# Optimization experiments

Measured on AMD Instinct MI355X. Metric: run time of the kernel, lower is better.

## Reference

```python
import jax, jax.numpy as jnp
import numpy as np

V, BLK, H, D, L = 32000, 1024, 16, 1024, 3
HD = D // H  # 64
B, T = 4, 1024


def _layernorm(x, g, b, eps=1e-5):
    mu = jnp.mean(x, axis=-1, keepdims=True)
    var = jnp.mean(jnp.square(x - mu), axis=-1, keepdims=True)
    return (x - mu) * jax.lax.rsqrt(var + eps) * g + b


def setup_inputs() -> dict:
    key = jax.random.key(0)
    ks = jax.random.split(key, 32)
    s = 0.02
    inp = {}
    inp["idx"] = jax.random.randint(ks[0], (B, T), 0, V)
    inp["target"] = jax.random.randint(ks[1], (B, T), 0, V)
    inp["tok_emb"] = jax.random.normal(ks[2], (V, D), jnp.float32) * s
    inp["pos_emb"] = jax.random.normal(ks[3], (BLK, D), jnp.float32) * s
    inp["wq"] = jax.random.normal(ks[4], (L, H, D, HD), jnp.float32) * s
    inp["wk"] = jax.random.normal(ks[5], (L, H, D, HD), jnp.float32) * s
    inp["wv"] = jax.random.normal(ks[6], (L, H, D, HD), jnp.float32) * s
    inp["wproj"] = jax.random.normal(ks[7], (L, D, D), jnp.float32) * s
    inp["bproj"] = jnp.zeros((L, D), jnp.float32)
    inp["ln1_g"] = jnp.ones((L, D), jnp.float32)
    inp["ln1_b"] = jnp.zeros((L, D), jnp.float32)
    inp["ln2_g"] = jnp.ones((L, D), jnp.float32)
    inp["ln2_b"] = jnp.zeros((L, D), jnp.float32)
    inp["w1"] = jax.random.normal(ks[8], (L, D, 4 * D), jnp.float32) * s
    inp["b1"] = jnp.zeros((L, 4 * D), jnp.float32)
    inp["w2"] = jax.random.normal(ks[9], (L, 4 * D, D), jnp.float32) * s
    inp["b2"] = jnp.zeros((L, D), jnp.float32)
    inp["lnf_g"] = jnp.ones((D,), jnp.float32)
    inp["lnf_b"] = jnp.zeros((D,), jnp.float32)
    inp["wlm"] = jax.random.normal(ks[10], (D, V), jnp.float32) * s
    inp["blm"] = jnp.zeros((V,), jnp.float32)
    return inp


def reference(idx, target, tok_emb, pos_emb, wq, wk, wv, wproj, bproj,
              ln1_g, ln1_b, ln2_g, ln2_b, w1, b1, w2, b2,
              lnf_g, lnf_b, wlm, blm):
    Bb, Tt = idx.shape
    x = tok_emb[idx] + pos_emb[:Tt]  # [B,T,D]
    mask = jnp.tril(jnp.ones((Tt, Tt), dtype=bool))  # causal
    scale = D ** -0.5  # NOTE: source scales by n_embd**-0.5, not head_size**-0.5
    for l in range(L):
        xn = _layernorm(x, ln1_g[l], ln1_b[l])
        q = jnp.einsum('btd,hde->bhte', xn, wq[l])
        k = jnp.einsum('btd,hde->bhte', xn, wk[l])
        v = jnp.einsum('btd,hde->bhte', xn, wv[l])
        scores = jnp.einsum('bhte,bhse->bhts', q, k) * scale
        scores = jnp.where(mask, scores, -jnp.inf)
        attn = jax.nn.softmax(scores, axis=-1)
        o = jnp.einsum('bhts,bhse->bhte', attn, v)
        o = o.transpose(0, 2, 1, 3).reshape(Bb, Tt, D)  # concat heads
        x = x + o @ wproj[l] + bproj[l]
        xn2 = _layernorm(x, ln2_g[l], ln2_b[l])
        h = jax.nn.relu(xn2 @ w1[l] + b1[l])
        x = x + h @ w2[l] + b2[l]
    x = _layernorm(x, lnf_g, lnf_b)
    logits = x @ wlm + blm  # [B,T,V]
    logp = jax.nn.log_softmax(logits, axis=-1)
    nll = -jnp.take_along_axis(logp, target[..., None], axis=-1)[..., 0]
    loss = jnp.mean(nll)
    return logits, loss
```

## Files before the change

kernel.cpp:

```cpp
#include <hip/hip_runtime.h>
#include <math.h>

#define Dn   1024
#define Hn   16
#define HDn  64
#define Tn   1024
#define Bn   4
#define Vn   32000
#define Ln   3
#define NT   (Bn*Tn)

typedef __attribute__((ext_vector_type(8))) short bf16x8;
typedef __attribute__((ext_vector_type(4))) float f32x4;

__device__ __forceinline__ float b2f(unsigned short u) {
  union { float f; unsigned int i; } c; c.i = ((unsigned int)u) << 16; return c.f;
}
__device__ __forceinline__ unsigned short f2b(float f) {
  union { float f; unsigned int i; } c; c.f = f;
  unsigned int r = (c.i + 0x7FFFu + ((c.i >> 16) & 1u)) >> 16;
  return (unsigned short)r;
}

#define GLOAD_LDS16(g, l) __builtin_amdgcn_global_load_lds( \
    (const __attribute__((address_space(1))) void*)(g),     \
    (__attribute__((address_space(3))) void*)(l), 16, 0, 0)

#define SBAR()  __builtin_amdgcn_s_barrier()
#define SCHED() __builtin_amdgcn_sched_barrier(0)

__global__ __launch_bounds__(256) void embed_kernel(
    const int* __restrict__ idx, const float* __restrict__ tok,
    const float* __restrict__ pos, float* __restrict__ x) {
  int row = blockIdx.x;
  int t = row & (Tn - 1);
  int token = idx[row];
  const float4* tp = (const float4*)(tok + (size_t)token * Dn);
  const float4* pp = (const float4*)(pos + (size_t)t * Dn);
  float4* xp = (float4*)(x + (size_t)row * Dn);
  int i = threadIdx.x;
  float4 a = tp[i], b = pp[i];
  xp[i] = make_float4(a.x + b.x, a.y + b.y, a.z + b.z, a.w + b.w);
}

__global__ __launch_bounds__(256) void ln_kernel(
    const float* __restrict__ x, const float* __restrict__ g,
    const float* __restrict__ b, unsigned short* __restrict__ y) {
  int row = blockIdx.x;
  const float4* xr = (const float4*)(x + (size_t)row * Dn);
  __shared__ float red[4];
  int lane = threadIdx.x & 63, w = threadIdx.x >> 6;

  float4 v = xr[threadIdx.x];
  float s = v.x + v.y + v.z + v.w;
  #pragma unroll
  for (int o = 32; o > 0; o >>= 1) s += __shfl_down(s, o, 64);
  if (lane == 0) red[w] = s;
  __syncthreads();
  float mu = (red[0] + red[1] + red[2] + red[3]) * (1.0f / Dn);
  __syncthreads();

  float dx = v.x - mu, dy = v.y - mu, dz = v.z - mu, dw = v.w - mu;
  float ss = dx*dx + dy*dy + dz*dz + dw*dw;
  #pragma unroll
  for (int o = 32; o > 0; o >>= 1) ss += __shfl_down(ss, o, 64);
  if (lane == 0) red[w] = ss;
  __syncthreads();
  float var = (red[0] + red[1] + red[2] + red[3]) * (1.0f / Dn);
  float inv = rsqrtf(var + 1e-5f);

  float4 gv = ((const float4*)g)[threadIdx.x];
  float4 bv = ((const float4*)b)[threadIdx.x];
  ushort4 o4;
  o4.x = f2b(dx*inv*gv.x + bv.x);
  o4.y = f2b(dy*inv*gv.y + bv.y);
  o4.z = f2b(dz*inv*gv.z + bv.z);
  o4.w = f2b(dw*inv*gv.w + bv.w);
  ((ushort4*)(y + (size_t)row * Dn))[threadIdx.x] = o4;
}

__global__ __launch_bounds__(256) void wcast_kernel(
    const float* __restrict__ src, unsigned short* __restrict__ dst,
    int K, int M, long long bsk, long long bsh) {
  __shared__ float t[32][33];
  int m0 = blockIdx.x << 5, k0 = blockIdx.y << 5;
  int tid = threadIdx.x;
  int ml = tid & 31, kl = tid >> 5;
  #pragma unroll
  for (int p = 0; p < 4; ++p) {
    int k = k0 + kl + p * 8;
    int m = m0 + ml;
    t[ml][kl + p * 8] = src[(size_t)k * bsk + (size_t)(m >> 6) * bsh + (m & 63)];
  }
  __syncthreads();
  int kl2 = tid & 31, ml2 = tid >> 5;
  #pragma unroll
  for (int p = 0; p < 4; ++p) {
    int m = m0 + ml2 + p * 8;
    int k = k0 + kl2;
    dst[(size_t)m * K + k] = f2b(t[ml2 + p * 8][kl2]);
  }
}

__global__ __launch_bounds__(256) void mm_bf16(
    const unsigned short* __restrict__ A, const unsigned short* __restrict__ BT,
    const float* __restrict__ bias, const float* __restrict__ res,
    float* __restrict__ Cf, unsigned short* __restrict__ Ch,
    int N, int K, int M, int relu) {
  __shared__ __align__(16) unsigned short As[2][128 * 32];
  __shared__ __align__(16) unsigned short Bs[2][128 * 32];
  const int tid = threadIdx.x;
  const int lane = tid & 63, w = tid >> 6, g = lane >> 4;
  const int wr = w >> 1, wc = w & 1;
  const int n0 = blockIdx.x << 7, m0 = blockIdx.y << 7;

  f32x4 acc[4][4];
  #pragma unroll
  for (int i = 0; i < 4; ++i)
    #pragma unroll
    for (int j = 0; j < 4; ++j)
      acc[i][j] = (f32x4){0.f, 0.f, 0.f, 0.f};

  const int beta0 = w * 2048 + lane * 16;
  const int beta1 = beta0 + 1024;
  const int r0 = beta0 >> 6, u0 = (beta0 >> 4) & 3;
  const int r1 = beta1 >> 6, u1 = (beta1 >> 4) & 3;
  const int ks0 = u0 ^ ((r0 >> 1) & 3);
  const int ks1 = u1 ^ ((r1 >> 1) & 3);
  const unsigned short* a_g0 = A + (size_t)(n0 + r0) * K + ks0 * 8;
  const unsigned short* a_g1 = A + (size_t)(n0 + r1) * K + ks1 * 8;
  const unsigned short* b_g0 = BT + (size_t)(m0 + r0) * K + ks0 * 8;
  const unsigned short* b_g1 = BT + (size_t)(m0 + r1) * K + ks1 * 8;

  int a_off[4], b_off[4];
  #pragma unroll
  for (int f = 0; f < 4; ++f) {
    int row = wr * 64 + f * 16 + (lane & 15);
    a_off[f] = row * 64 + ((g ^ ((row >> 1) & 3)) << 4);
    int col = wc * 64 + f * 16 + (lane & 15);
    b_off[f] = col * 64 + ((g ^ ((col >> 1) & 3)) << 4);
  }

#define MM_STAGE(buf, kk) do {                                   \
    GLOAD_LDS16(a_g0 + (kk), As[buf] + w * 1024);                \
    GLOAD_LDS16(a_g1 + (kk), As[buf] + w * 1024 + 512);          \
    GLOAD_LDS16(b_g0 + (kk), Bs[buf] + w * 1024);                \
    GLOAD_LDS16(b_g1 + (kk), Bs[buf] + w * 1024 + 512); } while (0)

#define MM_COMPUTE(buf) do {                                     \
    bf16x8 af[4], bfr[4];                                        \
    _Pragma("unroll")                                            \
    for (int f = 0; f < 4; ++f) {                                \
      af[f]  = *(const bf16x8*)((const char*)As[buf] + a_off[f]);\
      bfr[f] = *(const bf16x8*)((const char*)Bs[buf] + b_off[f]);\
    }                                                            \
    _Pragma("unroll")                                            \
    for (int i = 0; i < 4; ++i)                                  \
      _Pragma("unroll")                                          \
      for (int j = 0; j < 4; ++j)                                \
        acc[i][j] = __builtin_amdgcn_mfma_f32_16x16x32_bf16(af[i], bfr[j], acc[i][j], 0, 0, 0); } while (0)

  MM_STAGE(0, 0);
  int cur = 0;
  for (int k0 = 0; k0 < K - 32; k0 += 32) {
    MM_STAGE(cur ^ 1, k0 + 32);
    asm volatile("s_waitcnt vmcnt(4)" ::: "memory");
    SCHED(); SBAR(); SCHED();
    MM_COMPUTE(cur);
    SCHED(); SBAR(); SCHED();
    cur ^= 1;
  }
  asm volatile("s_waitcnt vmcnt(0)" ::: "memory");
  SCHED(); SBAR(); SCHED();
  MM_COMPUTE(cur);

  #pragma unroll
  for (int fc = 0; fc < 4; ++fc) {
    int colg = m0 + wc * 64 + fc * 16 + (lane & 15);
    float bz = bias ? bias[colg] : 0.f;
    #pragma unroll
    for (int fr = 0; fr < 4; ++fr) {
      #pragma unroll
      for (int i = 0; i < 4; ++i) {
        int rowg = n0 + wr * 64 + fr * 16 + (g << 2) + i;
        float v = acc[fr][fc][i] + bz;
        if (res) v += res[(size_t)rowg * M + colg];
        if (relu) v = fmaxf(v, 0.f);
        if (Cf) Cf[(size_t)rowg * M + colg] = v;
        else    Ch[(size_t)rowg * M + colg] = f2b(v);
      }
    }
  }
#undef MM_STAGE
#undef MM_COMPUTE
}

template<int OMODE>
__global__ __launch_bounds__(512) void mm512_bf16(
    const unsigned short* __restrict__ A, const unsigned short* __restrict__ BT,
    const float* __restrict__ bias, const float* __restrict__ res,
    float* __restrict__ Cf, unsigned short* __restrict__ Ch,
    float* __restrict__ rowsum, int N, int K, int M, int relu) {
  __shared__ __align__(16) unsigned short As[2][128 * 32];
  __shared__ __align__(16) unsigned short Bs[2][256 * 32];
  __shared__ float rsum2[OMODE == 4 ? 128 * 4 : 4];
  const int tid = threadIdx.x;
  const int lane = tid & 63, w = tid >> 6, g = lane >> 4;
  const int wr = w >> 2, wc = w & 3;
  const int n0 = blockIdx.x << 7, m0 = blockIdx.y << 8;

  f32x4 acc[4][4];
  #pragma unroll
  for (int i = 0; i < 4; ++i)
    #pragma unroll
    for (int j = 0; j < 4; ++j)
      acc[i][j] = (f32x4){0.f, 0.f, 0.f, 0.f};

  const int arow = tid >> 2, au = tid & 3;
  const int aks = au ^ ((arow >> 1) & 3);
  const unsigned short* a_g = A + (size_t)(n0 + arow) * K + aks * 8;
  const int brow1 = (tid + 512) >> 2;
  const int bks0 = au ^ ((arow >> 1) & 3);
  const int bks1 = au ^ ((brow1 >> 1) & 3);
  const unsigned short* b_g0 = BT + (size_t)(m0 + arow) * K + bks0 * 8;
  const unsigned short* b_g1 = BT + (size_t)(m0 + brow1) * K + bks1 * 8;

  int a_off[4], b_off[4];
  #pragma unroll
  for (int f = 0; f < 4; ++f) {
    int row = wr * 64 + f * 16 + (lane & 15);
    a_off[f] = row * 64 + ((g ^ ((row >> 1) & 3)) << 4);
    int col = wc * 64 + f * 16 + (lane & 15);
    b_off[f] = col * 64 + ((g ^ ((col >> 1) & 3)) << 4);
  }

#define MM5_STAGE(buf, kk) do {                                  \
    GLOAD_LDS16(a_g + (kk), As[buf] + tid * 8);                  \
    GLOAD_LDS16(b_g0 + (kk), Bs[buf] + tid * 8);                 \
    GLOAD_LDS16(b_g1 + (kk), Bs[buf] + (tid + 512) * 8); } while (0)

#define MM5_COMPUTE(buf) do {                                    \
    bf16x8 af[4], bfr[4];                                        \
    _Pragma("unroll")                                            \
    for (int f = 0; f < 4; ++f) {                                \
      af[f]  = *(const bf16x8*)((const char*)As[buf] + a_off[f]);\
      bfr[f] = *(const bf16x8*)((const char*)Bs[buf] + b_off[f]);\
    }                                                            \
    _Pragma("unroll")                                            \
    for (int i = 0; i < 4; ++i)                                  \
      _Pragma("unroll")                                          \
      for (int j = 0; j < 4; ++j)                                \
        acc[i][j] = __builtin_amdgcn_mfma_f32_16x16x32_bf16(af[i], bfr[j], acc[i][j], 0, 0, 0); } while (0)

  MM5_STAGE(0, 0);
  int cur = 0;
  for (int k0 = 0; k0 < K - 32; k0 += 32) {
    MM5_STAGE(cur ^ 1, k0 + 32);
    asm volatile("s_waitcnt vmcnt(3)" ::: "memory");
    SCHED(); SBAR(); SCHED();
    MM5_COMPUTE(cur);
    SCHED(); SBAR(); SCHED();
    cur ^= 1;
  }
  asm volatile("s_waitcnt vmcnt(0)" ::: "memory");
  SCHED(); SBAR(); SCHED();
  MM5_COMPUTE(cur);

  if (OMODE == 0) {
    #pragma unroll
    for (int fc = 0; fc < 4; ++fc) {
      int colg = m0 + wc * 64 + fc * 16 + (lane & 15);
      float bz = bias ? bias[colg] : 0.f;
      #pragma unroll
      for (int fr = 0; fr < 4; ++fr) {
        #pragma unroll
        for (int i = 0; i < 4; ++i) {
          int rowg = n0 + wr * 64 + fr * 16 + (g << 2) + i;
          float v = acc[fr][fc][i] + bz;
          if (res) v += res[(size_t)rowg * M + colg];
          if (relu) v = fmaxf(v, 0.f);
          if (Cf) Cf[(size_t)rowg * M + colg] = v;
          else    Ch[(size_t)rowg * M + colg] = f2b(v);
        }
      }
    }
  } else if (OMODE == 3) {
    unsigned short* kb  = Ch + (size_t)NT * Dn;
    unsigned short* vtb = Ch + 2 * (size_t)NT * Dn;
    #pragma unroll
    for (int fc = 0; fc < 4; ++fc) {
      int colg = m0 + wc * 64 + fc * 16 + (lane & 15);
      int sel = colg >> 10, hh = (colg >> 6) & 15, e = colg & 63;
      #pragma unroll
      for (int fr = 0; fr < 4; ++fr) {
        int rowg0 = n0 + wr * 64 + fr * 16 + (g << 2);
        int b = rowg0 >> 10, t0 = rowg0 & 1023;
        if (sel == 2) {
          ushort4 pk;
          pk.x = f2b(acc[fr][fc][0]); pk.y = f2b(acc[fr][fc][1]);
          pk.z = f2b(acc[fr][fc][2]); pk.w = f2b(acc[fr][fc][3]);
          *(ushort4*)&vtb[(((size_t)(b * 16 + hh) * 64) + e) * 1024 + t0] = pk;
        } else {
          unsigned short* dst = (sel == 0) ? Ch : kb;
          #pragma unroll
          for (int i = 0; i < 4; ++i)
            dst[(((size_t)(b * 16 + hh) * 1024) + t0 + i) * 64 + e] = f2b(acc[fr][fc][i]);
        }
      }
    }
  } else {
    #pragma unroll
    for (int fr = 0; fr < 4; ++fr) {
      #pragma unroll
      for (int i = 0; i < 4; ++i) {
        int rloc = wr * 64 + fr * 16 + (g << 2) + i;
        int rowg = n0 + rloc;
        float es = 0.f;
        #pragma unroll
        for (int fc = 0; fc < 4; ++fc) {
          int colg = m0 + wc * 64 + fc * 16 + (lane & 15);
          float v = acc[fr][fc][i] + bias[colg];
          __builtin_nontemporal_store(v, &Cf[(size_t)rowg * M + colg]);
          es += __expf(v);
        }
        es += __shfl_xor(es, 1); es += __shfl_xor(es, 2);
        es += __shfl_xor(es, 4); es += __shfl_xor(es, 8);
        if ((lane & 15) == 0) rsum2[rloc * 4 + wc] = es;
      }
    }
    __syncthreads();
    if (tid < 128)
      atomicAdd(&rowsum[n0 + tid],
                rsum2[tid * 4 + 0] + rsum2[tid * 4 + 1] +
                rsum2[tid * 4 + 2] + rsum2[tid * 4 + 3]);
  }
#undef MM5_STAGE
#undef MM5_COMPUTE
}

__global__ __launch_bounds__(256) void fattn_kernel(
    const unsigned short* __restrict__ qg, const unsigned short* __restrict__ kg,
    const unsigned short* __restrict__ vtg, unsigned short* __restrict__ ob) {
  const int bid = blockIdx.x;
  const int qt = bid & 15, bh = bid >> 4;
  const int b = bh >> 4, h = bh & 15;
  const int tid = threadIdx.x, lane = tid & 63, w = tid >> 6, g = lane >> 4;

  __shared__ __align__(16) unsigned short Ks[2][64 * 64];
  __shared__ __align__(16) unsigned short Vs[2][64 * 64];
  __shared__ __align__(16) unsigned short Pb[4][16 * 64];

  const unsigned short* kbase = kg + (size_t)bh * Tn * HDn;
  const unsigned short* vbase = vtg + (size_t)bh * HDn * Tn;

  const int qrow = qt * 64 + w * 16 + (lane & 15);
  const unsigned short* qptr = qg + ((size_t)bh * Tn + qrow) * HDn;
  bf16x8 qf0 = *(const bf16x8*)(qptr + g * 8);
  bf16x8 qf1 = *(const bf16x8*)(qptr + 32 + g * 8);

  f32x4 accO[4];
  #pragma unroll
  for (int dt = 0; dt < 4; ++dt) accO[dt] = (f32x4){0.f, 0.f, 0.f, 0.f};
  float mrun[4] = {-1e30f, -1e30f, -1e30f, -1e30f};
  float lrun[4] = {0.f, 0.f, 0.f, 0.f};

  const float scale = 0.03125f;
  const int qout0 = qt * 64 + w * 16 + 4 * g;

  unsigned short* pb = &Pb[w][0];
  const int nsteps = qt + 1;

#define FA_STAGE(buf, s0_) do {                                              \
    _Pragma("unroll")                                                        \
    for (int r = 0; r < 2; ++r) {                                            \
      int c = tid + 256 * r;                                                 \
      int srow = c >> 3, u = c & 7;                                          \
      GLOAD_LDS16(kbase + (size_t)((s0_) + srow) * HDn + ((u ^ (srow & 7)) * 8), Ks[buf] + c * 8); \
    }                                                                        \
    _Pragma("unroll")                                                        \
    for (int r = 0; r < 2; ++r) {                                            \
      int c = tid + 256 * r;                                                 \
      int d = c >> 3, u = c & 7;                                             \
      GLOAD_LDS16(vbase + (size_t)d * Tn + (s0_) + ((u ^ (d & 7)) * 8), Vs[buf] + c * 8); \
    } } while (0)

  FA_STAGE(0, 0);
  int cur = 0;

  for (int st = 0; st < nsteps; ++st) {
    const int s0 = st * 64;
    if (st + 1 < nsteps) {
      FA_STAGE(cur ^ 1, s0 + 64);
      asm volatile("s_waitcnt vmcnt(4)" ::: "memory");
    } else {
      asm volatile("s_waitcnt vmcnt(0)" ::: "memory");
    }
    SCHED(); SBAR(); SCHED();

    float p[4][4];
    #pragma unroll
    for (int sub = 0; sub < 4; ++sub) {
      int srow = sub * 16 + (lane & 15);
      const char* kr = (const char*)Ks[cur] + srow * 128;
      bf16x8 kf0 = *(const bf16x8*)(kr + ((g ^ (srow & 7)) * 16));
      bf16x8 kf1 = *(const bf16x8*)(kr + (((4 + g) ^ (srow & 7)) * 16));
      f32x4 s4 = (f32x4){0.f, 0.f, 0.f, 0.f};
      s4 = __builtin_amdgcn_mfma_f32_16x16x32_bf16(qf0, kf0, s4, 0, 0, 0);
      s4 = __builtin_amdgcn_mfma_f32_16x16x32_bf16(qf1, kf1, s4, 0, 0, 0);
      int sg = s0 + srow;
      #pragma unroll
      for (int i = 0; i < 4; ++i)
        p[sub][i] = (sg > qout0 + i) ? -1e30f : s4[i] * scale;
    }

    #pragma unroll
    for (int i = 0; i < 4; ++i) {
      float v = fmaxf(fmaxf(p[0][i], p[1][i]), fmaxf(p[2][i], p[3][i]));
      v = fmaxf(v, __shfl_xor(v, 1)); v = fmaxf(v, __shfl_xor(v, 2));
      v = fmaxf(v, __shfl_xor(v, 4)); v = fmaxf(v, __shfl_xor(v, 8));
      float nm = fmaxf(mrun[i], v);
      float fac = __expf(mrun[i] - nm);
      mrun[i] = nm;
      #pragma unroll
      for (int dt = 0; dt < 4; ++dt) accO[dt][i] *= fac;
      float sum = 0.f;
      #pragma unroll
      for (int sub = 0; sub < 4; ++sub) {
        float e = __expf(p[sub][i] - nm);
        p[sub][i] = e;
        sum += e;
      }
      sum += __shfl_xor(sum, 1); sum += __shfl_xor(sum, 2);
      sum += __shfl_xor(sum, 4); sum += __shfl_xor(sum, 8);
      lrun[i] = lrun[i] * fac + sum;
    }

    #pragma unroll
    for (int sub = 0; sub < 4; ++sub) {
      int s = sub * 16 + (lane & 15);
      #pragma unroll
      for (int i = 0; i < 4; ++i) {
        int q = 4 * g + i;
        pb[q * 64 + (((s >> 3) ^ (q & 7)) * 8) + (s & 7)] = f2b(p[sub][i]);
      }
    }

    #pragma unroll
    for (int sc = 0; sc < 2; ++sc) {
      int qq = lane & 15;
      bf16x8 pa = *(const bf16x8*)((const char*)pb + qq * 128 + (((sc * 4 + g) ^ (qq & 7)) * 16));
      #pragma unroll
      for (int dt = 0; dt < 4; ++dt) {
        int d = dt * 16 + (lane & 15);
        bf16x8 vf = *(const bf16x8*)((const char*)Vs[cur] + d * 128 + (((sc * 4 + g) ^ (d & 7)) * 16));
        accO[dt] = __builtin_amdgcn_mfma_f32_16x16x32_bf16(pa, vf, accO[dt], 0, 0, 0);
      }
    }

    SCHED(); SBAR(); SCHED();
    cur ^= 1;
  }
#undef FA_STAGE

  float rinv[4];
  #pragma unroll
  for (int i = 0; i < 4; ++i) rinv[i] = 1.0f / lrun[i];
  #pragma unroll
  for (int dt = 0; dt < 4; ++dt) {
    int dcol = h * 64 + dt * 16 + (lane & 15);
    #pragma unroll
    for (int i = 0; i < 4; ++i) {
      int t = qout0 + i;
      ob[((size_t)(b * Tn + t)) * Dn + dcol] = f2b(accO[dt][i] * rinv[i]);
    }
  }
}

__global__ __launch_bounds__(256) void loss_kernel(
    const float* __restrict__ logits, const float* __restrict__ rowsum,
    const int* __restrict__ target, float* __restrict__ out_loss) {
  __shared__ float red[4];
  int lane = threadIdx.x & 63, w = threadIdx.x >> 6;
  float s = 0.f;
  for (int row = threadIdx.x; row < NT; row += 256) {
    float lt = logits[(size_t)row * Vn + target[row]];
    s += logf(rowsum[row]) - lt;
  }
  #pragma unroll
  for (int off = 32; off > 0; off >>= 1) s += __shfl_down(s, off, 64);
  if (lane == 0) red[w] = s;
  __syncthreads();
  if (threadIdx.x == 0)
    *out_loss = (red[0] + red[1] + red[2] + red[3]) * (1.0f / NT);
}

static inline void launch_wcast(const float* src, unsigned short* dst, int K, int M,
                                long long bsk, long long bsh, hipStream_t s) {
  dim3 g(M >> 5, K >> 5);
  wcast_kernel<<<g, 256, 0, s>>>(src, dst, K, M, bsk, bsh);
}

static inline void launch_mm(const unsigned short* A, const unsigned short* BT,
                             const float* bias, const float* res,
                             float* Cf, unsigned short* Ch,
                             int N, int K, int M, int relu, hipStream_t s) {
  dim3 g(N >> 7, M >> 7);
  mm_bf16<<<g, 256, 0, s>>>(A, BT, bias, res, Cf, Ch, N, K, M, relu);
}

template<int OMODE>
static inline void launch_mm512(const unsigned short* A, const unsigned short* BT,
                                const float* bias, const float* res,
                                float* Cf, unsigned short* Ch, float* rowsum,
                                int N, int K, int M, int relu, hipStream_t s) {
  dim3 g(N >> 7, M >> 8);
  mm512_bf16<OMODE><<<g, 512, 0, s>>>(A, BT, bias, res, Cf, Ch, rowsum, N, K, M, relu);
}

extern "C" void kernel_launch(void* const* d_in, const int* in_sizes, int n_in,
                              void* d_out, int out_size, void* d_ws, size_t ws_size,
                              hipStream_t stream) {
  const int*   idx    = (const int*)d_in[0];
  const int*   target = (const int*)d_in[1];
  const float* tok    = (const float*)d_in[2];
  const float* pos    = (const float*)d_in[3];
  const float* wq     = (const float*)d_in[4];
  const float* wk     = (const float*)d_in[5];
  const float* wv     = (const float*)d_in[6];
  const float* wproj  = (const float*)d_in[7];
  const float* bproj  = (const float*)d_in[8];
  const float* ln1g   = (const float*)d_in[9];
  const float* ln1b   = (const float*)d_in[10];
  const float* ln2g   = (const float*)d_in[11];
  const float* ln2b   = (const float*)d_in[12];
  const float* w1     = (const float*)d_in[13];
  const float* b1     = (const float*)d_in[14];
  const float* w2     = (const float*)d_in[15];
  const float* b2     = (const float*)d_in[16];
  const float* lnfg   = (const float*)d_in[17];
  const float* lnfb   = (const float*)d_in[18];
  const float* wlm    = (const float*)d_in[19];
  const float* blm    = (const float*)d_in[20];

  float* out = (float*)d_out;

  char* p = (char*)d_ws;
  float* x  = (float*)p;                 p += (size_t)NT * Dn * 4;
  unsigned short* xn = (unsigned short*)p; p += (size_t)NT * Dn * 2;
  unsigned short* reg = (unsigned short*)p; p += (size_t)NT * 4 * Dn * 2;
  unsigned short* wT = (unsigned short*)p; p += (size_t)Vn * Dn * 2;
  float* rowsum = (float*)p;

  unsigned short* qb  = reg;
  unsigned short* kb  = reg + (size_t)NT * Dn;
  unsigned short* vtb = reg + 2 * (size_t)NT * Dn;
  unsigned short* ob  = reg + 3 * (size_t)NT * Dn;
  unsigned short* hb  = reg;

  embed_kernel<<<NT, 256, 0, stream>>>(idx, tok, pos, x);

  for (int l = 0; l < Ln; ++l) {
    const float* wq_l = wq + (size_t)l * Hn * Dn * HDn;
    const float* wk_l = wk + (size_t)l * Hn * Dn * HDn;
    const float* wv_l = wv + (size_t)l * Hn * Dn * HDn;

    ln_kernel<<<NT, 256, 0, stream>>>(x, ln1g + l * Dn, ln1b + l * Dn, xn);

    launch_wcast(wq_l, wT,                  Dn, Dn, HDn, (long long)Dn * HDn, stream);
    launch_wcast(wk_l, wT + 1024 * Dn,      Dn, Dn, HDn, (long long)Dn * HDn, stream);
    launch_wcast(wv_l, wT + 2048 * Dn,      Dn, Dn, HDn, (long long)Dn * HDn, stream);
    launch_mm512<3>(xn, wT, nullptr, nullptr, nullptr, qb, nullptr, NT, Dn, 3072, 0, stream);

    fattn_kernel<<<Bn * Hn * (Tn / 64), 256, 0, stream>>>(qb, kb, vtb, ob);

    launch_wcast(wproj + (size_t)l * Dn * Dn, wT, Dn, Dn, Dn, 64, stream);
    launch_mm(ob, wT, bproj + l * Dn, x, x, nullptr, NT, Dn, Dn, 0, stream);

    ln_kernel<<<NT, 256, 0, stream>>>(x, ln2g + l * Dn, ln2b + l * Dn, xn);

    launch_wcast(w1 + (size_t)l * Dn * 4 * Dn, wT, Dn, 4 * Dn, 4 * Dn, 64, stream);
    launch_mm512<0>(xn, wT, b1 + l * 4 * Dn, nullptr, nullptr, hb, nullptr, NT, Dn, 4 * Dn, 1, stream);
    launch_wcast(w2 + (size_t)l * 4 * Dn * Dn, wT, 4 * Dn, Dn, Dn, 64, stream);
    launch_mm(hb, wT, b2 + l * Dn, x, x, nullptr, NT, 4 * Dn, Dn, 0, stream);
  }

  ln_kernel<<<NT, 256, 0, stream>>>(x, lnfg, lnfb, xn);

  hipMemsetAsync(rowsum, 0, NT * sizeof(float), stream);
  launch_wcast(wlm, wT, Dn, Vn, Vn, 64, stream);
  launch_mm512<4>(xn, wT, blm, nullptr, out, nullptr, rowsum, NT, Dn, Vn, 0, stream);

  loss_kernel<<<1, 256, 0, stream>>>(out, rowsum, target, out + (size_t)NT * Vn);
}
```

Before: 1.275 ms.

## Triple-buffer LDS tiles in bf16 GEMM kernels for deeper prefetch

Both GEMM kernels go from double to triple buffering of the A/B LDS tiles. Each iteration now issues global-to-LDS loads two k-steps ahead and adjusts the vmcnt waits to match, so memory latency is better hidden behind MFMA work. LDS use per block grows by half, which can lower occupancy, most of all for the 512-thread kernel with its 256-wide B tile. The ring-index bookkeeping and branchy tail waits also add a little control overhead.

```diff
diff --git a/kernel.cpp b/kernel.cpp
--- a/kernel.cpp
+++ b/kernel.cpp
@@ -107,8 +107,8 @@
     const float* __restrict__ bias, const float* __restrict__ res,
     float* __restrict__ Cf, unsigned short* __restrict__ Ch,
     int N, int K, int M, int relu) {
-  __shared__ __align__(16) unsigned short As[2][128 * 32];
-  __shared__ __align__(16) unsigned short Bs[2][128 * 32];
+  __shared__ __align__(16) unsigned short As[3][128 * 32];
+  __shared__ __align__(16) unsigned short Bs[3][128 * 32];
   const int tid = threadIdx.x;
   const int lane = tid & 63, w = tid >> 6, g = lane >> 4;
   const int wr = w >> 1, wc = w & 1;
@@ -161,18 +161,23 @@
         acc[i][j] = __builtin_amdgcn_mfma_f32_16x16x32_bf16(af[i], bfr[j], acc[i][j], 0, 0, 0); } while (0)
 
   MM_STAGE(0, 0);
-  int cur = 0;
-  for (int k0 = 0; k0 < K - 32; k0 += 32) {
-    MM_STAGE(cur ^ 1, k0 + 32);
-    asm volatile("s_waitcnt vmcnt(4)" ::: "memory");
+  MM_STAGE(1, 32);
+  int bc = 0, bp = 2;
+  for (int k0 = 0; k0 < K; k0 += 32) {
+    if (k0 + 64 < K) {
+      MM_STAGE(bp, k0 + 64);
+      asm volatile("s_waitcnt vmcnt(8)" ::: "memory");
+    } else if (k0 + 32 < K) {
+      asm volatile("s_waitcnt vmcnt(4)" ::: "memory");
+    } else {
+      asm volatile("s_waitcnt vmcnt(0)" ::: "memory");
+    }
     SCHED(); SBAR(); SCHED();
-    MM_COMPUTE(cur);
+    MM_COMPUTE(bc);
     SCHED(); SBAR(); SCHED();
-    cur ^= 1;
-  }
-  asm volatile("s_waitcnt vmcnt(0)" ::: "memory");
-  SCHED(); SBAR(); SCHED();
-  MM_COMPUTE(cur);
+    bc = (bc == 2) ? 0 : bc + 1;
+    bp = (bp == 2) ? 0 : bp + 1;
+  }
 
   #pragma unroll
   for (int fc = 0; fc < 4; ++fc) {
@@ -201,8 +206,8 @@
     const float* __restrict__ bias, const float* __restrict__ res,
     float* __restrict__ Cf, unsigned short* __restrict__ Ch,
     float* __restrict__ rowsum, int N, int K, int M, int relu) {
-  __shared__ __align__(16) unsigned short As[2][128 * 32];
-  __shared__ __align__(16) unsigned short Bs[2][256 * 32];
+  __shared__ __align__(16) unsigned short As[3][128 * 32];
+  __shared__ __align__(16) unsigned short Bs[3][256 * 32];
   __shared__ float rsum2[OMODE == 4 ? 128 * 4 : 4];
   const int tid = threadIdx.x;
   const int lane = tid & 63, w = tid >> 6, g = lane >> 4;
@@ -253,18 +258,23 @@
         acc[i][j] = __builtin_amdgcn_mfma_f32_16x16x32_bf16(af[i], bfr[j], acc[i][j], 0, 0, 0); } while (0)
 
   MM5_STAGE(0, 0);
-  int cur = 0;
-  for (int k0 = 0; k0 < K - 32; k0 += 32) {
-    MM5_STAGE(cur ^ 1, k0 + 32);
-    asm volatile("s_waitcnt vmcnt(3)" ::: "memory");
+  MM5_STAGE(1, 32);
+  int bc = 0, bp = 2;
+  for (int k0 = 0; k0 < K; k0 += 32) {
+    if (k0 + 64 < K) {
+      MM5_STAGE(bp, k0 + 64);
+      asm volatile("s_waitcnt vmcnt(6)" ::: "memory");
+    } else if (k0 + 32 < K) {
+      asm volatile("s_waitcnt vmcnt(3)" ::: "memory");
+    } else {
+      asm volatile("s_waitcnt vmcnt(0)" ::: "memory");
+    }
     SCHED(); SBAR(); SCHED();
-    MM5_COMPUTE(cur);
+    MM5_COMPUTE(bc);
     SCHED(); SBAR(); SCHED();
-    cur ^= 1;
-  }
-  asm volatile("s_waitcnt vmcnt(0)" ::: "memory");
-  SCHED(); SBAR(); SCHED();
-  MM5_COMPUTE(cur);
+    bc = (bc == 2) ? 0 : bc + 1;
+    bp = (bp == 2) ? 0 : bp + 1;
+  }
 
   if (OMODE == 0) {
     #pragma unroll
```

New measurement: 1.291 ms. No clear change (+1.3%).
